# Kernel tuning notes

Hardware: AMD Instinct MI355X
Metric: run time of the kernel (lower is better)

The kernel has to match this reference:

```python
import jax, jax.numpy as jnp
import numpy as np

B, C, H, WID = 32, 64, 128, 128
K = 5            # co-occurrence bins (co_shape)
WH = 3           # spatial filter height/width (w_shape = (1,3,3), depth 1)
ACT_LO, ACT_HI = 0.0, 1.0  # actBounds


def setup_inputs() -> dict:
    key = jax.random.key(0)
    k1, k2, k3 = jax.random.split(key, 3)
    input_tensor = jax.random.uniform(k1, (B, C, H, WID), dtype=jnp.float32)
    # learned params: L ~ N(0, 0.1) of shape (k,k); W ~ N(0,0.1) of shape (d,h,w)
    L = 0.1 * jax.random.normal(k2, (K, K), dtype=jnp.float32)
    W = 0.1 * jax.random.normal(k3, (1, WH, WH), dtype=jnp.float32)
    return {"input_tensor": input_tensor, "W": W, "L": L}


def _quantize(x, k):
    # map activation in [ACT_LO, ACT_HI] to bin index in [0, k-1]
    b = jnp.floor((x - ACT_LO) / (ACT_HI - ACT_LO) * k)
    return jnp.clip(b, 0, k - 1).astype(jnp.int32)


def reference(input_tensor, W, L):
    """Co-occurrence layer:
    out[p] = sum_{q in 3x3 nbhd(p)} W[q-p] * L[bin(x[q]), bin(x[p])] * x[q]
    Out-of-bounds neighbors contribute 0 (zero pad => x[q]=0 kills the term),
    matching the precomputed neighbor_lookup_table boundary handling.
    """
    k = L.shape[0]
    pad = WH // 2
    bins = _quantize(input_tensor, k)                      # (B,C,H,W) int32
    xp = jnp.pad(input_tensor, ((0, 0), (0, 0), (pad, pad), (pad, pad)))
    bp = jnp.pad(bins, ((0, 0), (0, 0), (pad, pad), (pad, pad)))
    h, w = input_tensor.shape[2], input_tensor.shape[3]
    out = jnp.zeros_like(input_tensor)
    for dh in range(WH):                                   # tiny fixed 3x3 loop
        for dw in range(WH):
            xn = xp[:, :, dh:dh + h, dw:dw + w]            # shifted neighbor values
            bn = bp[:, :, dh:dh + h, dw:dw + w]            # shifted neighbor bins
            out = out + W[0, dh, dw] * L[bn, bins] * xn    # gather L + weighted acc
    return out
```

## Files before the change

### kernel.cpp

```cpp
#include <hip/hip_runtime.h>


namespace {
constexpr int H  = 128;
constexpr int WD = 128;
constexpr int PLANES = 32 * 64;
constexpr int ROWS_PER_BLOCK = 16;
constexpr int TILES_PER_PLANE = H / ROWS_PER_BLOCK;
constexpr int THREADS = ROWS_PER_BLOCK * (WD / 4);
}

__global__ __launch_bounds__(THREADS) void col_kernel(
    const float* __restrict__ x, const float* __restrict__ Wf,
    const float* __restrict__ Lf, float* __restrict__ out)
{
    __shared__ float Ls[32];
    const int t = threadIdx.x;
    if (t < 25) Ls[t] = Lf[t];

    float w[9];
    #pragma unroll
    for (int i = 0; i < 9; ++i) w[i] = Wf[i];

    __syncthreads();

    const int bid   = blockIdx.x;
    const int plane = bid >> 3;
    const int tile  = bid & 7;
    const int row   = tile * ROWS_PER_BLOCK + (t >> 5);
    const int col0  = (t & 31) << 2;

    const float* xp = x + (size_t)plane * (H * WD);

    float win[3][6];
    #pragma unroll
    for (int dr = 0; dr < 3; ++dr) {
        const int rr = row + dr - 1;
        const bool vr = (rr >= 0) && (rr < H);
        const float* rp = xp + rr * WD + col0;
        float4 c = make_float4(0.f, 0.f, 0.f, 0.f);
        float l = 0.f, r = 0.f;
        if (vr) {
            c = *(const float4*)rp;
            if (col0 > 0)      l = rp[-1];
            if (col0 < WD - 4) r = rp[4];
        }
        win[dr][0] = l;   win[dr][1] = c.x; win[dr][2] = c.y;
        win[dr][3] = c.z; win[dr][4] = c.w; win[dr][5] = r;
    }

    int bq[3][6];
    #pragma unroll
    for (int dr = 0; dr < 3; ++dr) {
        #pragma unroll
        for (int i = 0; i < 6; ++i) {
            int b = (int)(win[dr][i] * 5.0f);
            bq[dr][i] = (b > 4) ? 4 : b;
        }
    }

    int bp[4];
    #pragma unroll
    for (int i = 0; i < 4; ++i) bp[i] = bq[1][i + 1];

    float acc[4] = {0.f, 0.f, 0.f, 0.f};
    #pragma unroll
    for (int dr = 0; dr < 3; ++dr) {
        #pragma unroll
        for (int dw = 0; dw < 3; ++dw) {
            const float wv = w[dr * 3 + dw];
            #pragma unroll
            for (int i = 0; i < 4; ++i) {
                const float xqv = win[dr][i + dw];
                const float lv  = Ls[bq[dr][i + dw] * 5 + bp[i]];
                acc[i] = fmaf(wv * xqv, lv, acc[i]);
            }
        }
    }

    float* op = out + (size_t)plane * (H * WD) + row * WD + col0;
    *(float4*)op = make_float4(acc[0], acc[1], acc[2], acc[3]);
}

extern "C" void kernel_launch(void* const* d_in, const int* in_sizes, int n_in,
                              void* d_out, int out_size, void* d_ws, size_t ws_size,
                              hipStream_t stream) {
    const float* x  = (const float*)d_in[0];
    const float* Wf = (const float*)d_in[1];
    const float* Lf = (const float*)d_in[2];
    float* out = (float*)d_out;

    col_kernel<<<dim3(PLANES * TILES_PER_PLANE), dim3(THREADS), 0, stream>>>(
        x, Wf, Lf, out);
}
```

Before: 261.7 us.

## Premultiply W into L table and compute 8 pixels per thread

Builds a 9x25 shared-memory table holding W times L, so the per-tap multiply by the weight disappears. Lookups use precomputed byte offsets (bin*20 + bin*4 + tap*100) to cut index arithmetic. Each thread now handles 8 columns instead of 4, which halves the thread count per block and raises reuse of the loaded neighbour halo. The cost is more registers per thread and a 225-entry table fill at block start.

```diff
diff --git a/kernel.cpp b/kernel.cpp
--- a/kernel.cpp
+++ b/kernel.cpp
@@ -6,80 +6,82 @@
 constexpr int WD = 128;
 constexpr int PLANES = 32 * 64;
 constexpr int ROWS_PER_BLOCK = 16;
-constexpr int TILES_PER_PLANE = H / ROWS_PER_BLOCK;
-constexpr int THREADS = ROWS_PER_BLOCK * (WD / 4);
+constexpr int PX = 8;
+constexpr int THREADS = ROWS_PER_BLOCK * (WD / PX);
+constexpr int TILES = H / ROWS_PER_BLOCK;
 }
 
 __global__ __launch_bounds__(THREADS) void col_kernel(
     const float* __restrict__ x, const float* __restrict__ Wf,
     const float* __restrict__ Lf, float* __restrict__ out)
 {
-    __shared__ float Ls[32];
+    __shared__ float WL[9 * 25];
     const int t = threadIdx.x;
-    if (t < 25) Ls[t] = Lf[t];
-
-    float w[9];
-    #pragma unroll
-    for (int i = 0; i < 9; ++i) w[i] = Wf[i];
-
+    if (t < 225) WL[t] = Wf[t / 25] * Lf[t % 25];
     __syncthreads();
 
-    const int bid   = blockIdx.x;
-    const int plane = bid >> 3;
-    const int tile  = bid & 7;
-    const int row   = tile * ROWS_PER_BLOCK + (t >> 5);
-    const int col0  = (t & 31) << 2;
+    const int plane = blockIdx.x >> 3;
+    const int tile  = blockIdx.x & 7;
+    const int row   = tile * ROWS_PER_BLOCK + (t >> 4);
+    const int col0  = (t & 15) * PX;
 
     const float* xp = x + (size_t)plane * (H * WD);
 
-    float win[3][6];
+    float win[3][PX + 2];
     #pragma unroll
     for (int dr = 0; dr < 3; ++dr) {
         const int rr = row + dr - 1;
         const bool vr = (rr >= 0) && (rr < H);
         const float* rp = xp + rr * WD + col0;
-        float4 c = make_float4(0.f, 0.f, 0.f, 0.f);
+        float4 c0 = make_float4(0.f, 0.f, 0.f, 0.f);
+        float4 c1 = make_float4(0.f, 0.f, 0.f, 0.f);
         float l = 0.f, r = 0.f;
         if (vr) {
-            c = *(const float4*)rp;
-            if (col0 > 0)      l = rp[-1];
-            if (col0 < WD - 4) r = rp[4];
+            c0 = *(const float4*)rp;
+            c1 = *(const float4*)(rp + 4);
+            if (col0 > 0)       l = rp[-1];
+            if (col0 < WD - PX) r = rp[PX];
         }
-        win[dr][0] = l;   win[dr][1] = c.x; win[dr][2] = c.y;
-        win[dr][3] = c.z; win[dr][4] = c.w; win[dr][5] = r;
+        win[dr][0] = l;
+        win[dr][1] = c0.x; win[dr][2] = c0.y; win[dr][3] = c0.z; win[dr][4] = c0.w;
+        win[dr][5] = c1.x; win[dr][6] = c1.y; win[dr][7] = c1.z; win[dr][8] = c1.w;
+        win[dr][9] = r;
     }
 
-    int bq[3][6];
+    int bq20[3][PX + 2];
+    int bp4[PX];
     #pragma unroll
     for (int dr = 0; dr < 3; ++dr) {
         #pragma unroll
-        for (int i = 0; i < 6; ++i) {
-            int b = (int)(win[dr][i] * 5.0f);
-            bq[dr][i] = (b > 4) ? 4 : b;
+        for (int j = 0; j < PX + 2; ++j) {
+            int b = (int)(win[dr][j] * 5.0f);
+            b = (b > 4) ? 4 : b;
+            bq20[dr][j] = b * 20;
+            if (dr == 1 && j >= 1 && j <= PX) bp4[j - 1] = b * 4;
         }
     }
 
-    int bp[4];
+    const char* wlb = (const char*)WL;
+    float acc[PX];
     #pragma unroll
-    for (int i = 0; i < 4; ++i) bp[i] = bq[1][i + 1];
+    for (int i = 0; i < PX; ++i) acc[i] = 0.f;
 
-    float acc[4] = {0.f, 0.f, 0.f, 0.f};
     #pragma unroll
     for (int dr = 0; dr < 3; ++dr) {
         #pragma unroll
         for (int dw = 0; dw < 3; ++dw) {
-            const float wv = w[dr * 3 + dw];
             #pragma unroll
-            for (int i = 0; i < 4; ++i) {
-                const float xqv = win[dr][i + dw];
-                const float lv  = Ls[bq[dr][i + dw] * 5 + bp[i]];
-                acc[i] = fmaf(wv * xqv, lv, acc[i]);
+            for (int i = 0; i < PX; ++i) {
+                const float lw = *(const float*)(
+                    wlb + (bq20[dr][i + dw] + bp4[i] + (dr * 3 + dw) * 100));
+                acc[i] = fmaf(lw, win[dr][i + dw], acc[i]);
             }
         }
     }
 
     float* op = out + (size_t)plane * (H * WD) + row * WD + col0;
-    *(float4*)op = make_float4(acc[0], acc[1], acc[2], acc[3]);
+    *(float4*)op       = make_float4(acc[0], acc[1], acc[2], acc[3]);
+    *(float4*)(op + 4) = make_float4(acc[4], acc[5], acc[6], acc[7]);
 }
 
 extern "C" void kernel_launch(void* const* d_in, const int* in_sizes, int n_in,
@@ -90,6 +92,5 @@
     const float* Lf = (const float*)d_in[2];
     float* out = (float*)d_out;
 
-    col_kernel<<<dim3(PLANES * TILES_PER_PLANE), dim3(THREADS), 0, stream>>>(
-        x, Wf, Lf, out);
+    col_kernel<<<dim3(PLANES * TILES), dim3(THREADS), 0, stream>>>(x, Wf, Lf, out);
 }
```

New measurement: 256.0 us. 2.2% less time.
